# Performance work log

Hardware: AMD Instinct MI355X
Metric: run time of the kernel (lower is better)

The kernel has to match this reference:

```python
import jax, jax.numpy as jnp
import numpy as np

B, L, HID, TRANS = 16384, 512, 768, 128


def setup_inputs() -> dict:
    key = jax.random.key(0)
    ks = jax.random.split(key, 12)
    def lin(k, out_d, in_d):
        kw, kb = jax.random.split(k)
        s = 1.0 / np.sqrt(in_d)
        return (jax.random.uniform(kw, (out_d, in_d), jnp.float32, -s, s),
                jax.random.uniform(kb, (out_d,), jnp.float32, -s, s))
    W_text, b_text = lin(ks[0], TRANS, HID)
    W_label, b_label = lin(ks[1], TRANS, HID)
    W0, b0 = lin(ks[2], TRANS, 2 * TRANS)
    W1, b1 = lin(ks[3], TRANS, TRANS)
    W2, b2 = lin(ks[4], 1, TRANS)
    target = jax.random.randint(ks[5], (B, L), 0, 2, jnp.int32)
    # guarantee every sample has at least one positive label (torch.mean on empty would NaN)
    target = target.at[:, 0].set(1)
    return {
        "text_embed": jax.random.normal(ks[6], (B, HID), jnp.float32),
        "label_embed": jax.random.normal(ks[7], (L, HID), jnp.float32),
        "target": target,
        "perm": jax.random.permutation(ks[8], B).astype(jnp.int32),
        "W_text": W_text, "b_text": b_text,
        "W_label": W_label, "b_label": b_label,
        "W0": W0, "b0": b0, "W1": W1, "b1": b1, "W2": W2, "b2": b2,
    }


def _network(t, l, W_text, b_text, W_label, b_label, W0, b0, W1, b1, W2, b2):
    tt = t @ W_text.T + b_text            # [B, trans]
    ll = l @ W_label.T + b_label          # [B, trans]
    h = jnp.concatenate([tt, ll], axis=1)  # [B, 2*trans]
    h = jax.nn.relu(h @ W0.T + b0)
    h = jax.nn.relu(h @ W1.T + b1)
    return h @ W2.T + b2                  # [B, 1]


def reference(text_embed, label_embed, target, perm,
              W_text, b_text, W_label, b_label, W0, b0, W1, b1, W2, b2):
    # variable-length mean pooling of label embeddings selected by the multi-hot target
    mask = target.astype(text_embed.dtype)                 # [B, L]
    counts = jnp.maximum(mask.sum(axis=1, keepdims=True), 1.0)
    label_feature_y = (mask @ label_embed) / counts        # [B, hid]
    negative_text = text_embed[perm]                       # shuffled negatives
    params = (W_text, b_text, W_label, b_label, W0, b0, W1, b1, W2, b2)
    E_joint = -jnp.mean(jax.nn.softplus(-_network(text_embed, label_feature_y, *params)))
    E_marginal = jnp.mean(jax.nn.softplus(_network(negative_text, label_feature_y, *params)))
    return E_marginal - E_joint
```

## Files before the change

kernel.cpp:

```cpp
#include <hip/hip_runtime.h>
#include <math.h>

#define BATCH 16384
#define LBL   512
#define HID   768
#define TR    128

typedef unsigned long long u64;
typedef unsigned short ushort_t;
typedef __attribute__((ext_vector_type(8))) short short8;
typedef __attribute__((ext_vector_type(4))) float f32x4;

__device__ __forceinline__ ushort_t f2bf(float f){
  unsigned u = __builtin_bit_cast(unsigned, f);
  u += 0x7FFFu + ((u >> 16) & 1u);
  return (ushort_t)(u >> 16);
}
__device__ __forceinline__ float bf2f(ushort_t h){
  unsigned u = ((unsigned)h) << 16;
  return __builtin_bit_cast(float, u);
}
__device__ __forceinline__ float softplusf(float x){
  return fmaxf(x, 0.0f) + log1pf(expf(-fabsf(x)));
}
__device__ __forceinline__ void gload_lds16(const void* g, void* l){
  __builtin_amdgcn_global_load_lds((const __attribute__((address_space(1))) void*)g,
                                   (__attribute__((address_space(3))) void*)l, 16, 0, 0);
}

__global__ __launch_bounds__(256) void k1(
    const float* __restrict__ W0, const float* __restrict__ Wt, const float* __restrict__ Wl,
    const float* __restrict__ bt, const float* __restrict__ bl, const float* __restrict__ b0,
    const float* __restrict__ W1,
    ushort_t* __restrict__ Msw, ushort_t* __restrict__ Qsw, ushort_t* __restrict__ W1B,
    float* __restrict__ KV, float* __restrict__ out){
  __shared__ float sw[TR];
  int bi = blockIdx.x, t = threadIdx.x;
  if (bi < 256){
    int i = bi & 127;
    int isQ = bi >> 7;
    const float* src = isQ ? Wl : Wt;
    ushort_t* dst = isQ ? Qsw : Msw;
    if (t < TR) sw[t] = W0[(size_t)i*256 + isQ*128 + t];
    if (!isQ && t < 128) W1B[i*128 + t] = f2bf(W1[i*128 + t]);
    __syncthreads();
    int c = t;
    float a0 = 0.f, a1 = 0.f, a2 = 0.f;
    #pragma unroll 8
    for (int a = 0; a < 128; a++){
      float w = sw[a];
      const float* r = src + (size_t)a*HID;
      a0 = fmaf(w, r[c], a0);
      a1 = fmaf(w, r[c+256], a1);
      a2 = fmaf(w, r[c+512], a2);
    }
    int c7 = c & 7;
    dst[(((c      )>>3)<<10) + (i<<3) + c7] = f2bf(a0);
    dst[(((c + 256)>>3)<<10) + (i<<3) + c7] = f2bf(a1);
    dst[(((c + 512)>>3)<<10) + (i<<3) + c7] = f2bf(a2);
  } else {
    if (t < TR){
      float s = b0[t];
      const float* r = W0 + (size_t)t*256;
      for (int a = 0; a < 128; a++) s = fmaf(r[a], bt[a], s);
      for (int a = 0; a < 128; a++) s = fmaf(r[128+a], bl[a], s);
      KV[t] = s;
    }
    if (t == 0) out[0] = 0.f;
  }
}

__global__ __launch_bounds__(256) void k2(
    const float* __restrict__ labe, const ushort_t* __restrict__ Qsw,
    const float* __restrict__ T,    const ushort_t* __restrict__ Msw,
    const float* __restrict__ KV,
    ushort_t* __restrict__ Gt, ushort_t* __restrict__ U){
  __shared__ __align__(16) ushort_t Bs[2][8192];
  __shared__ __align__(16) ushort_t As[2][16][72];
  int bi = blockIdx.x, tid = threadIdx.x;
  int lane = tid & 63, wave = tid >> 6;
  int m = lane & 15, q = lane >> 4;
  int arow = tid >> 4, a4 = (tid & 15) * 4;

  if (bi < 32){
    int l0 = bi * 16;
    const float* ap = labe + (size_t)(l0 + arow)*HID + a4;
    float4 ra = *(const float4*)ap;
    {
      const char* gb = (const char*)Qsw;
      char* lb = (char*)&Bs[0][0];
      #pragma unroll
      for (int p = 0; p < 4; p++)
        gload_lds16(gb + p*4096 + tid*16, lb + p*4096 + tid*16);
    }
    f32x4 acc[2] = {{0,0,0,0},{0,0,0,0}};
    for (int c = 0; c < 12; c++){
      int buf = c & 1;
      ushort_t* ad = &As[buf][arow][a4];
      ad[0]=f2bf(ra.x); ad[1]=f2bf(ra.y); ad[2]=f2bf(ra.z); ad[3]=f2bf(ra.w);
      __syncthreads();
      if (c < 11){
        ra = *(const float4*)(ap + (c+1)*64);
        const char* gb = (const char*)Qsw + (size_t)(c+1)*16384;
        char* lb = (char*)&Bs[buf^1][0];
        #pragma unroll
        for (int p = 0; p < 4; p++)
          gload_lds16(gb + p*4096 + tid*16, lb + p*4096 + tid*16);
      }
      #pragma unroll
      for (int kcc = 0; kcc < 2; kcc++){
        short8 a = *(const short8*)&As[buf][m][kcc*32 + q*8];
        #pragma unroll
        for (int ct = 0; ct < 2; ct++){
          int col = wave*32 + ct*16 + m;
          short8 b = *(const short8*)&Bs[buf][(kcc*4 + q)*1024 + col*8];
          acc[ct] = __builtin_amdgcn_mfma_f32_16x16x32_bf16(a, b, acc[ct], 0, 0, 0);
        }
      }
    }
    __syncthreads();
    ushort_t (*GTs)[24] = (ushort_t(*)[24])&Bs[0][0];
    #pragma unroll
    for (int ct = 0; ct < 2; ct++){
      int col = wave*32 + ct*16 + m;
      #pragma unroll
      for (int r = 0; r < 4; r++)
        GTs[col][q*4 + r] = f2bf(acc[ct][r]);
    }
    __syncthreads();
    int gi = tid >> 1, loff = (tid & 1) * 8;
    *(short8*)(Gt + (size_t)gi*LBL + l0 + loff) = *(const short8*)&GTs[gi][loff];
  } else {
    int r0 = (bi - 32) * 16;
    const float* ap = T + (size_t)(r0 + arow)*HID + a4;
    float4 ra = *(const float4*)ap;
    {
      const char* gb = (const char*)Msw;
      char* lb = (char*)&Bs[0][0];
      #pragma unroll
      for (int p = 0; p < 4; p++)
        gload_lds16(gb + p*4096 + tid*16, lb + p*4096 + tid*16);
    }
    f32x4 acc[2] = {{0,0,0,0},{0,0,0,0}};
    for (int c = 0; c < 12; c++){
      int buf = c & 1;
      ushort_t* ad = &As[buf][arow][a4];
      ad[0]=f2bf(ra.x); ad[1]=f2bf(ra.y); ad[2]=f2bf(ra.z); ad[3]=f2bf(ra.w);
      __syncthreads();
      if (c < 11){
        ra = *(const float4*)(ap + (c+1)*64);
        const char* gb = (const char*)Msw + (size_t)(c+1)*16384;
        char* lb = (char*)&Bs[buf^1][0];
        #pragma unroll
        for (int p = 0; p < 4; p++)
          gload_lds16(gb + p*4096 + tid*16, lb + p*4096 + tid*16);
      }
      #pragma unroll
      for (int kcc = 0; kcc < 2; kcc++){
        short8 a = *(const short8*)&As[buf][m][kcc*32 + q*8];
        #pragma unroll
        for (int ct = 0; ct < 2; ct++){
          int col = wave*32 + ct*16 + m;
          short8 b = *(const short8*)&Bs[buf][(kcc*4 + q)*1024 + col*8];
          acc[ct] = __builtin_amdgcn_mfma_f32_16x16x32_bf16(a, b, acc[ct], 0, 0, 0);
        }
      }
    }
    #pragma unroll
    for (int ct = 0; ct < 2; ct++){
      int col = wave*32 + ct*16 + m;
      float kv = KV[col];
      #pragma unroll
      for (int r = 0; r < 4; r++)
        U[(size_t)(r0 + q*4 + r)*TR + col] = f2bf(acc[ct][r] + kv);
    }
  }
}

__global__ __launch_bounds__(256) void k3(const ushort_t* __restrict__ U, const ushort_t* __restrict__ Gt,
                                          const int* __restrict__ tgt, const int* __restrict__ perm,
                                          const ushort_t* __restrict__ W1b, const float* __restrict__ b1,
                                          const float* __restrict__ W2, const float* __restrict__ b2,
                                          float* __restrict__ out){
  __shared__ __align__(16) u64 bits_s8[16*10];
  __shared__ __align__(16) ushort_t h0s[32][136];
  __shared__ float sred[4][2][16][17];
  __shared__ float invs[16];
  __shared__ int   permS[16];

  int tid = threadIdx.x;
  int lane = tid & 63, wave = tid >> 6;
  int m = lane & 15, q = lane >> 4;
  int r0 = blockIdx.x * 16;

  if (tid < 16) permS[tid] = perm[r0 + tid];

  #pragma unroll
  for (int rr = 0; rr < 4; rr++){
    int row = wave*4 + rr;
    const int* rp = tgt + (size_t)(r0 + row)*LBL;
    int v[8];
    #pragma unroll
    for (int c = 0; c < 8; c++) v[c] = rp[c*64 + lane];
    int cnt = 0;
    #pragma unroll
    for (int c = 0; c < 8; c++){
      u64 mm = __ballot(v[c] != 0);
      if (lane == 0){ bits_s8[row*10 + c] = mm; cnt += __popcll(mm); }
    }
    if (lane == 0) invs[row] = 1.0f / (float)(cnt < 1 ? 1 : cnt);
  }
  __syncthreads();

  float up[2][4], un[2][4];
  #pragma unroll
  for (int ct = 0; ct < 2; ct++){
    int col = wave*32 + ct*16 + m;
    #pragma unroll
    for (int r = 0; r < 4; r++){
      int rowl = q*4 + r;
      up[ct][r] = bf2f(U[(size_t)(r0 + rowl)*TR + col]);
      un[ct][r] = bf2f(U[(size_t)permS[rowl]*TR + col]);
    }
  }

  const unsigned char* bits_b = (const unsigned char*)bits_s8;
  f32x4 accV[2] = {{0,0,0,0},{0,0,0,0}};
  const ushort_t* gp[2];
  #pragma unroll
  for (int ct = 0; ct < 2; ct++)
    gp[ct] = Gt + (size_t)(wave*32 + ct*16 + m)*LBL + q*8;
  short8 bcur[2], bnext[2];
  #pragma unroll
  for (int ct = 0; ct < 2; ct++) bcur[ct] = *(const short8*)(gp[ct]);
  int abase = m*80 + q;
  for (int c = 0; c < 16; c++){
    if (c < 15){
      #pragma unroll
      for (int ct = 0; ct < 2; ct++) bnext[ct] = *(const short8*)(gp[ct] + (c+1)*32);
    }
    unsigned bb = bits_b[abase + c*4];
    short8 a;
    #pragma unroll
    for (int j = 0; j < 8; j++) a[j] = (short)(((bb >> j) & 1u) ? 0x3F80 : 0);
    #pragma unroll
    for (int ct = 0; ct < 2; ct++)
      accV[ct] = __builtin_amdgcn_mfma_f32_16x16x32_bf16(a, bcur[ct], accV[ct], 0, 0, 0);
    #pragma unroll
    for (int ct = 0; ct < 2; ct++) bcur[ct] = bnext[ct];
  }

  #pragma unroll
  for (int ct = 0; ct < 2; ct++){
    int col = wave*32 + ct*16 + m;
    #pragma unroll
    for (int r = 0; r < 4; r++){
      int rowl = q*4 + r;
      float v = accV[ct][r] * invs[rowl];
      h0s[rowl][col]      = f2bf(fmaxf(up[ct][r] + v, 0.f));
      h0s[16 + rowl][col] = f2bf(fmaxf(un[ct][r] + v, 0.f));
    }
  }
  __syncthreads();

  float w2c[2], b1c[2];
  #pragma unroll
  for (int ct = 0; ct < 2; ct++){
    int col = wave*32 + ct*16 + m;
    w2c[ct] = W2[col];
    b1c[ct] = b1[col];
  }
  float b2v = b2[0];

  #pragma unroll
  for (int half = 0; half < 2; half++){
    f32x4 accH[2] = {{0,0,0,0},{0,0,0,0}};
    #pragma unroll
    for (int kc = 0; kc < 4; kc++){
      short8 a = *(const short8*)&h0s[half*16 + m][kc*32 + q*8];
      #pragma unroll
      for (int ct = 0; ct < 2; ct++){
        short8 b = *(const short8*)(W1b + (size_t)(wave*32 + ct*16 + m)*TR + kc*32 + q*8);
        accH[ct] = __builtin_amdgcn_mfma_f32_16x16x32_bf16(a, b, accH[ct], 0, 0, 0);
      }
    }
    #pragma unroll
    for (int r = 0; r < 4; r++){
      float sp = 0.f;
      #pragma unroll
      for (int ct = 0; ct < 2; ct++)
        sp = fmaf(w2c[ct], fmaxf(accH[ct][r] + b1c[ct], 0.f), sp);
      sred[wave][half][q*4 + r][m] = sp;
    }
  }
  __syncthreads();

  if (tid < 32){
    int half = tid >> 4, row = tid & 15;
    float s = b2v;
    #pragma unroll
    for (int wx = 0; wx < 4; wx++)
      #pragma unroll
      for (int n = 0; n < 16; n++) s += sred[wx][half][row][n];
    float val = half ? softplusf(s) : softplusf(-s);
    #pragma unroll
    for (int off = 16; off > 0; off >>= 1) val += __shfl_down(val, off);
    if (tid == 0) atomicAdd(out, val * (1.0f / (float)BATCH));
  }
}

extern "C" void kernel_launch(void* const* d_in, const int* in_sizes, int n_in,
                              void* d_out, int out_size, void* d_ws, size_t ws_size,
                              hipStream_t stream){
  const float* text = (const float*)d_in[0];
  const float* labe = (const float*)d_in[1];
  const int*   tgt  = (const int*)  d_in[2];
  const int*   perm = (const int*)  d_in[3];
  const float* Wt   = (const float*)d_in[4];
  const float* bt   = (const float*)d_in[5];
  const float* Wl   = (const float*)d_in[6];
  const float* bl   = (const float*)d_in[7];
  const float* W0   = (const float*)d_in[8];
  const float* b0   = (const float*)d_in[9];
  const float* W1   = (const float*)d_in[10];
  const float* b1   = (const float*)d_in[11];
  const float* W2   = (const float*)d_in[12];
  const float* b2   = (const float*)d_in[13];

  char* wsb = (char*)d_ws;
  size_t off = 0;
  auto alloc = [&](size_t bytes){
    size_t r = off;
    off += (bytes + 255) & ~(size_t)255;
    return r;
  };
  ushort_t* MSW = (ushort_t*)(wsb + alloc((size_t)TR*HID*2));
  ushort_t* QSW = (ushort_t*)(wsb + alloc((size_t)TR*HID*2));
  ushort_t* GT  = (ushort_t*)(wsb + alloc((size_t)TR*LBL*2));
  ushort_t* W1B = (ushort_t*)(wsb + alloc((size_t)TR*TR*2));
  float*    KV  = (float*)   (wsb + alloc((size_t)TR*4));
  ushort_t* U   = (ushort_t*)(wsb + alloc((size_t)BATCH*TR*2));
  (void)ws_size; (void)in_sizes; (void)n_in; (void)out_size;

  k1<<<257, 256, 0, stream>>>(W0, Wt, Wl, bt, bl, b0, W1, MSW, QSW, W1B, KV, (float*)d_out);
  k2<<<1056, 256, 0, stream>>>(labe, QSW, text, MSW, KV, GT, U);
  k3<<<BATCH/16, 256, 0, stream>>>(U, GT, tgt, perm, W1B, b1, W2, b2, (float*)d_out);
}
```

Baseline: 172.8 us.

## Fuse three kernels into one cooperative persistent kernel with grid syncs

Merges the weight-precompute, projection GEMM and MLP/loss kernels into a single cooperative kernel of 512 blocks (32 rows each) separated by two grid-wide barriers. The target bitmask loading now overlaps the weight-preparation phase, and each block keeps its U projection in registers instead of re-reading it. This removes two kernel launch boundaries and their tail effects. In exchange it adds grid.sync costs, caps the grid at two blocks per CU, and serializes the label GEMM onto only 16 blocks. It falls back to the old three-kernel path if occupancy is insufficient.

```diff
diff --git a/kernel.cpp b/kernel.cpp
--- a/kernel.cpp
+++ b/kernel.cpp
@@ -1,4 +1,5 @@
 #include <hip/hip_runtime.h>
+#include <hip/hip_cooperative_groups.h>
 #include <math.h>
 
 #define BATCH 16384
@@ -6,6 +7,8 @@
 #define HID   768
 #define TR    128
 
+namespace cg = cooperative_groups;
+
 typedef unsigned long long u64;
 typedef unsigned short ushort_t;
 typedef __attribute__((ext_vector_type(8))) short short8;
@@ -26,6 +29,286 @@
 __device__ __forceinline__ void gload_lds16(const void* g, void* l){
   __builtin_amdgcn_global_load_lds((const __attribute__((address_space(1))) void*)g,
                                    (__attribute__((address_space(3))) void*)l, 16, 0, 0);
+}
+
+
+__device__ __forceinline__ void gemm768_32(const float* ap, const ushort_t* Bsw,
+                                           ushort_t* As_, ushort_t* Bs_,
+                                           int tid, int wave, int m, int q,
+                                           f32x4 acc[2][2]){
+  int arow = tid >> 3, ak = (tid & 7) * 8;
+  (void)arow; (void)ak;
+  float4 ra0 = *(const float4*)ap;
+  float4 ra1 = *(const float4*)(ap + 4);
+  {
+    const char* gb = (const char*)Bsw;
+    char* lb = (char*)Bs_;
+    #pragma unroll
+    for (int p = 0; p < 4; p++)
+      gload_lds16(gb + p*4096 + tid*16, lb + p*4096 + tid*16);
+  }
+  #pragma unroll
+  for (int rt = 0; rt < 2; rt++)
+    #pragma unroll
+    for (int ct = 0; ct < 2; ct++)
+      acc[rt][ct] = (f32x4){0.f,0.f,0.f,0.f};
+
+  for (int c = 0; c < 12; c++){
+    int buf = c & 1;
+    short8 av;
+    av[0] = (short)f2bf(ra0.x); av[1] = (short)f2bf(ra0.y);
+    av[2] = (short)f2bf(ra0.z); av[3] = (short)f2bf(ra0.w);
+    av[4] = (short)f2bf(ra1.x); av[5] = (short)f2bf(ra1.y);
+    av[6] = (short)f2bf(ra1.z); av[7] = (short)f2bf(ra1.w);
+    *(short8*)(As_ + (size_t)(buf*32 + (tid >> 3))*80 + (tid & 7)*8) = av;
+    __syncthreads();
+    if (c < 11){
+      ra0 = *(const float4*)(ap + (c+1)*64);
+      ra1 = *(const float4*)(ap + (c+1)*64 + 4);
+      const char* gb = (const char*)Bsw + (size_t)(c+1)*16384;
+      char* lb = (char*)(Bs_ + (buf^1)*8192);
+      #pragma unroll
+      for (int p = 0; p < 4; p++)
+        gload_lds16(gb + p*4096 + tid*16, lb + p*4096 + tid*16);
+    }
+    #pragma unroll
+    for (int kcc = 0; kcc < 2; kcc++){
+      short8 bfr[2];
+      #pragma unroll
+      for (int ct = 0; ct < 2; ct++)
+        bfr[ct] = *(const short8*)(Bs_ + buf*8192 + (kcc*4 + q)*1024 + (wave*32 + ct*16 + m)*8);
+      #pragma unroll
+      for (int rt = 0; rt < 2; rt++){
+        short8 a = *(const short8*)(As_ + (size_t)(buf*32 + rt*16 + m)*80 + kcc*32 + q*8);
+        #pragma unroll
+        for (int ct = 0; ct < 2; ct++)
+          acc[rt][ct] = __builtin_amdgcn_mfma_f32_16x16x32_bf16(a, bfr[ct], acc[rt][ct], 0, 0, 0);
+      }
+    }
+  }
+}
+
+__global__ __launch_bounds__(256, 2) void kfused(
+    const float* __restrict__ W0, const float* __restrict__ Wt, const float* __restrict__ Wl,
+    const float* __restrict__ bt, const float* __restrict__ bl, const float* __restrict__ b0,
+    const float* __restrict__ W1, const float* __restrict__ T,  const float* __restrict__ labe,
+    const int* __restrict__ tgt,  const int* __restrict__ perm,
+    const float* __restrict__ b1, const float* __restrict__ W2, const float* __restrict__ b2,
+    ushort_t* __restrict__ Msw, ushort_t* __restrict__ Qsw, ushort_t* __restrict__ W1B,
+    float* __restrict__ KV, ushort_t* __restrict__ Gt, ushort_t* __restrict__ U,
+    float* __restrict__ out){
+  __shared__ __align__(16) char uni[43008];
+  __shared__ __align__(16) u64 bitsS[32*10];
+  __shared__ float invs[32];
+  __shared__ int   permS[32];
+
+  cg::grid_group grid = cg::this_grid();
+  int bi = blockIdx.x, tid = threadIdx.x;
+  int lane = tid & 63, wave = tid >> 6;
+  int m = lane & 15, q = lane >> 4;
+  int r0 = bi * 32;
+  int arow = tid >> 3, ak = (tid & 7) * 8;
+
+  if (tid < 32) permS[tid] = perm[r0 + tid];
+  #pragma unroll
+  for (int rr = 0; rr < 8; rr++){
+    int row = wave*8 + rr;
+    const int* rp = tgt + (size_t)(r0 + row)*LBL;
+    int v[8];
+    #pragma unroll
+    for (int c = 0; c < 8; c++) v[c] = rp[c*64 + lane];
+    int cnt = 0;
+    #pragma unroll
+    for (int c = 0; c < 8; c++){
+      u64 mm = __ballot(v[c] != 0);
+      if (lane == 0){ bitsS[row*10 + c] = mm; cnt += __popcll(mm); }
+    }
+    if (lane == 0) invs[row] = 1.0f / (float)(cnt < 1 ? 1 : cnt);
+  }
+
+  if (bi < 256){
+    int i = bi & 127;
+    int isQ = bi >> 7;
+    const float* src = isQ ? Wl : Wt;
+    ushort_t* dst = isQ ? Qsw : Msw;
+    float* sw = (float*)uni;
+    if (tid < TR) sw[tid] = W0[(size_t)i*256 + isQ*128 + tid];
+    if (!isQ && tid < 128) W1B[i*128 + tid] = f2bf(W1[i*128 + tid]);
+    __syncthreads();
+    int c = tid;
+    float a0 = 0.f, a1 = 0.f, a2 = 0.f;
+    #pragma unroll 8
+    for (int a = 0; a < 128; a++){
+      float w = sw[a];
+      const float* r = src + (size_t)a*HID;
+      a0 = fmaf(w, r[c], a0);
+      a1 = fmaf(w, r[c+256], a1);
+      a2 = fmaf(w, r[c+512], a2);
+    }
+    int c7 = c & 7;
+    dst[(((c      )>>3)<<10) + (i<<3) + c7] = f2bf(a0);
+    dst[(((c + 256)>>3)<<10) + (i<<3) + c7] = f2bf(a1);
+    dst[(((c + 512)>>3)<<10) + (i<<3) + c7] = f2bf(a2);
+  } else if (bi == 256){
+    if (tid < TR){
+      float s = b0[tid];
+      const float* r = W0 + (size_t)tid*256;
+      for (int a = 0; a < 128; a++) s = fmaf(r[a], bt[a], s);
+      for (int a = 0; a < 128; a++) s = fmaf(r[128+a], bl[a], s);
+      KV[tid] = s;
+    }
+    if (tid == 0) out[0] = 0.f;
+  }
+  __threadfence();
+  grid.sync();
+
+  ushort_t* Bs_ = (ushort_t*)uni;
+  ushort_t* As_ = (ushort_t*)(uni + 32768);
+
+  f32x4 accU[2][2];
+  gemm768_32(T + (size_t)(r0 + arow)*HID + ak, Msw, As_, Bs_, tid, wave, m, q, accU);
+
+  float upf[2][2][4];
+  #pragma unroll
+  for (int rt = 0; rt < 2; rt++)
+    #pragma unroll
+    for (int ct = 0; ct < 2; ct++){
+      int col = wave*32 + ct*16 + m;
+      float kv = KV[col];
+      #pragma unroll
+      for (int r = 0; r < 4; r++){
+        upf[rt][ct][r] = accU[rt][ct][r] + kv;
+        U[(size_t)(r0 + rt*16 + q*4 + r)*TR + col] = f2bf(upf[rt][ct][r]);
+      }
+    }
+
+  if (bi < 16){
+    int l0 = bi * 32;
+    f32x4 accG[2][2];
+    __syncthreads();
+    gemm768_32(labe + (size_t)(l0 + arow)*HID + ak, Qsw, As_, Bs_, tid, wave, m, q, accG);
+    __syncthreads();
+    ushort_t (*GTs)[40] = (ushort_t(*)[40])uni;
+    #pragma unroll
+    for (int rt = 0; rt < 2; rt++)
+      #pragma unroll
+      for (int ct = 0; ct < 2; ct++){
+        int col = wave*32 + ct*16 + m;
+        #pragma unroll
+        for (int r = 0; r < 4; r++)
+          GTs[col][rt*16 + q*4 + r] = f2bf(accG[rt][ct][r]);
+      }
+    __syncthreads();
+    int gi = tid >> 1, half = tid & 1;
+    ushort_t* dstp = Gt + (size_t)gi*LBL + l0 + half*16;
+    *(short8*)(dstp)     = *(const short8*)&GTs[gi][half*16];
+    *(short8*)(dstp + 8) = *(const short8*)&GTs[gi][half*16 + 8];
+  }
+  __threadfence();
+  grid.sync();
+
+  ushort_t (*h0s)[136] = (ushort_t(*)[136])uni;
+  float* sred = (float*)(uni + 17408);
+
+  float un[2][2][4];
+  #pragma unroll
+  for (int rt = 0; rt < 2; rt++)
+    #pragma unroll
+    for (int ct = 0; ct < 2; ct++){
+      int col = wave*32 + ct*16 + m;
+      #pragma unroll
+      for (int r = 0; r < 4; r++)
+        un[rt][ct][r] = bf2f(U[(size_t)permS[rt*16 + q*4 + r]*TR + col]);
+    }
+
+  const unsigned char* bits_b = (const unsigned char*)bitsS;
+  f32x4 accV[2][2] = {{{0,0,0,0},{0,0,0,0}},{{0,0,0,0},{0,0,0,0}}};
+  const ushort_t* gp[2];
+  #pragma unroll
+  for (int ct = 0; ct < 2; ct++)
+    gp[ct] = Gt + (size_t)(wave*32 + ct*16 + m)*LBL + q*8;
+  short8 bcur[2], bnext[2];
+  #pragma unroll
+  for (int ct = 0; ct < 2; ct++) bcur[ct] = *(const short8*)(gp[ct]);
+  for (int c = 0; c < 16; c++){
+    if (c < 15){
+      #pragma unroll
+      for (int ct = 0; ct < 2; ct++) bnext[ct] = *(const short8*)(gp[ct] + (c+1)*32);
+    }
+    #pragma unroll
+    for (int rt = 0; rt < 2; rt++){
+      unsigned bb = bits_b[(rt*16 + m)*80 + c*4 + q];
+      short8 a;
+      #pragma unroll
+      for (int j = 0; j < 8; j++) a[j] = (short)(((bb >> j) & 1u) ? 0x3F80 : 0);
+      #pragma unroll
+      for (int ct = 0; ct < 2; ct++)
+        accV[rt][ct] = __builtin_amdgcn_mfma_f32_16x16x32_bf16(a, bcur[ct], accV[rt][ct], 0, 0, 0);
+    }
+    #pragma unroll
+    for (int ct = 0; ct < 2; ct++) bcur[ct] = bnext[ct];
+  }
+
+  __syncthreads();
+  #pragma unroll
+  for (int rt = 0; rt < 2; rt++)
+    #pragma unroll
+    for (int ct = 0; ct < 2; ct++){
+      int col = wave*32 + ct*16 + m;
+      #pragma unroll
+      for (int r = 0; r < 4; r++){
+        int rowl = rt*16 + q*4 + r;
+        float v = accV[rt][ct][r] * invs[rowl];
+        h0s[rowl][col]      = f2bf(fmaxf(upf[rt][ct][r] + v, 0.f));
+        h0s[32 + rowl][col] = f2bf(fmaxf(un[rt][ct][r]  + v, 0.f));
+      }
+    }
+  __syncthreads();
+
+  float w2c[2], b1c[2];
+  #pragma unroll
+  for (int ct = 0; ct < 2; ct++){
+    int col = wave*32 + ct*16 + m;
+    w2c[ct] = W2[col];
+    b1c[ct] = b1[col];
+  }
+  float b2v = b2[0];
+
+  #pragma unroll
+  for (int rt2 = 0; rt2 < 4; rt2++){
+    f32x4 accH[2] = {{0,0,0,0},{0,0,0,0}};
+    #pragma unroll
+    for (int kc = 0; kc < 4; kc++){
+      short8 a = *(const short8*)&h0s[rt2*16 + m][kc*32 + q*8];
+      #pragma unroll
+      for (int ct = 0; ct < 2; ct++){
+        short8 b = *(const short8*)(W1B + (size_t)(wave*32 + ct*16 + m)*TR + kc*32 + q*8);
+        accH[ct] = __builtin_amdgcn_mfma_f32_16x16x32_bf16(a, b, accH[ct], 0, 0, 0);
+      }
+    }
+    #pragma unroll
+    for (int r = 0; r < 4; r++){
+      float sp = 0.f;
+      #pragma unroll
+      for (int ct = 0; ct < 2; ct++)
+        sp = fmaf(w2c[ct], fmaxf(accH[ct][r] + b1c[ct], 0.f), sp);
+      sred[((wave*4 + rt2)*16 + q*4 + r)*17 + m] = sp;
+    }
+  }
+  __syncthreads();
+
+  if (tid < 64){
+    int rt2 = tid >> 4, row = tid & 15;
+    float s = b2v;
+    #pragma unroll
+    for (int wx = 0; wx < 4; wx++)
+      #pragma unroll
+      for (int n = 0; n < 16; n++) s += sred[((wx*4 + rt2)*16 + row)*17 + n];
+    float val = (rt2 < 2) ? softplusf(-s) : softplusf(s);
+    #pragma unroll
+    for (int off = 32; off > 0; off >>= 1) val += __shfl_down(val, off);
+    if (tid == 0) atomicAdd(out, val * (1.0f / (float)BATCH));
+  }
 }
 
 __global__ __launch_bounds__(256) void k1(
@@ -194,7 +477,6 @@
   int r0 = blockIdx.x * 16;
 
   if (tid < 16) permS[tid] = perm[r0 + tid];
-
   #pragma unroll
   for (int rr = 0; rr < 4; rr++){
     int row = wave*4 + rr;
@@ -340,9 +622,24 @@
   ushort_t* W1B = (ushort_t*)(wsb + alloc((size_t)TR*TR*2));
   float*    KV  = (float*)   (wsb + alloc((size_t)TR*4));
   ushort_t* U   = (ushort_t*)(wsb + alloc((size_t)BATCH*TR*2));
+  float*    out = (float*)d_out;
   (void)ws_size; (void)in_sizes; (void)n_in; (void)out_size;
 
-  k1<<<257, 256, 0, stream>>>(W0, Wt, Wl, bt, bl, b0, W1, MSW, QSW, W1B, KV, (float*)d_out);
+  int occ = 0;
+  hipError_t qe = hipOccupancyMaxActiveBlocksPerMultiprocessor(&occ, (const void*)kfused, 256, 0);
+  if (qe == hipSuccess && occ >= 2){
+    void* args[] = {
+      (void*)&W0, (void*)&Wt, (void*)&Wl, (void*)&bt, (void*)&bl, (void*)&b0,
+      (void*)&W1, (void*)&text, (void*)&labe, (void*)&tgt, (void*)&perm,
+      (void*)&b1, (void*)&W2, (void*)&b2,
+      (void*)&MSW, (void*)&QSW, (void*)&W1B, (void*)&KV, (void*)&GT, (void*)&U,
+      (void*)&out
+    };
+    hipError_t e = hipLaunchCooperativeKernel((const void*)kfused, dim3(512), dim3(256), args, 0, stream);
+    if (e == hipSuccess) return;
+  }
+
+  k1<<<257, 256, 0, stream>>>(W0, Wt, Wl, bt, bl, b0, W1, MSW, QSW, W1B, KV, out);
   k2<<<1056, 256, 0, stream>>>(labe, QSW, text, MSW, KV, GT, U);
-  k3<<<BATCH/16, 256, 0, stream>>>(U, GT, tgt, perm, W1B, b1, W2, b2, (float*)d_out);
-}
+  k3<<<BATCH/16, 256, 0, stream>>>(U, GT, tgt, perm, W1B, b1, W2, b2, out);
+}
```

New measurement: 420.6 us. +143.4%, slower.

## Move target bitmask packing into k2 and double row tile to 32 in GEMMs

Applied to the files above, without the earlier changes.

Packing the multi-hot target rows into bitmasks and inverse counts moves from k3 into extra blocks of k2, so it runs concurrently with the text/label projection GEMMs and k3 only reads a compact bitmask. Both the k2 GEMMs and k3 now process 32 rows per block instead of 16, reusing each loaded weight tile across two row tiles of MFMAs. This halves the grid sizes, raises per-block register and LDS use, and adds a workspace round trip for bits and inverse counts.

```diff
diff --git a/kernel.cpp b/kernel.cpp
--- a/kernel.cpp
+++ b/kernel.cpp
@@ -70,162 +70,171 @@
   }
 }
 
+__device__ __forceinline__ void gemm768_32(const float* ap, const ushort_t* Bsw,
+                                           ushort_t* As_, ushort_t* Bs_,
+                                           int tid, int wave, int m, int q,
+                                           f32x4 acc[2][2]){
+  float4 ra0 = *(const float4*)ap;
+  float4 ra1 = *(const float4*)(ap + 4);
+  {
+    const char* gb = (const char*)Bsw;
+    char* lb = (char*)Bs_;
+    #pragma unroll
+    for (int p = 0; p < 4; p++)
+      gload_lds16(gb + p*4096 + tid*16, lb + p*4096 + tid*16);
+  }
+  #pragma unroll
+  for (int rt = 0; rt < 2; rt++)
+    #pragma unroll
+    for (int ct = 0; ct < 2; ct++)
+      acc[rt][ct] = (f32x4){0.f,0.f,0.f,0.f};
+
+  for (int c = 0; c < 12; c++){
+    int buf = c & 1;
+    short8 av;
+    av[0] = (short)f2bf(ra0.x); av[1] = (short)f2bf(ra0.y);
+    av[2] = (short)f2bf(ra0.z); av[3] = (short)f2bf(ra0.w);
+    av[4] = (short)f2bf(ra1.x); av[5] = (short)f2bf(ra1.y);
+    av[6] = (short)f2bf(ra1.z); av[7] = (short)f2bf(ra1.w);
+    *(short8*)(As_ + (size_t)(buf*32 + (tid >> 3))*80 + (tid & 7)*8) = av;
+    __syncthreads();
+    if (c < 11){
+      ra0 = *(const float4*)(ap + (c+1)*64);
+      ra1 = *(const float4*)(ap + (c+1)*64 + 4);
+      const char* gb = (const char*)Bsw + (size_t)(c+1)*16384;
+      char* lb = (char*)(Bs_ + (buf^1)*8192);
+      #pragma unroll
+      for (int p = 0; p < 4; p++)
+        gload_lds16(gb + p*4096 + tid*16, lb + p*4096 + tid*16);
+    }
+    #pragma unroll
+    for (int kcc = 0; kcc < 2; kcc++){
+      short8 bfr[2];
+      #pragma unroll
+      for (int ct = 0; ct < 2; ct++)
+        bfr[ct] = *(const short8*)(Bs_ + buf*8192 + (kcc*4 + q)*1024 + (wave*32 + ct*16 + m)*8);
+      #pragma unroll
+      for (int rt = 0; rt < 2; rt++){
+        short8 a = *(const short8*)(As_ + (size_t)(buf*32 + rt*16 + m)*80 + kcc*32 + q*8);
+        #pragma unroll
+        for (int ct = 0; ct < 2; ct++)
+          acc[rt][ct] = __builtin_amdgcn_mfma_f32_16x16x32_bf16(a, bfr[ct], acc[rt][ct], 0, 0, 0);
+      }
+    }
+  }
+}
+
 __global__ __launch_bounds__(256) void k2(
     const float* __restrict__ labe, const ushort_t* __restrict__ Qsw,
     const float* __restrict__ T,    const ushort_t* __restrict__ Msw,
-    const float* __restrict__ KV,
-    ushort_t* __restrict__ Gt, ushort_t* __restrict__ U){
-  __shared__ __align__(16) ushort_t Bs[2][8192];
-  __shared__ __align__(16) ushort_t As[2][16][72];
+    const float* __restrict__ KV,   const int* __restrict__ tgt,
+    ushort_t* __restrict__ Gt, ushort_t* __restrict__ U,
+    u64* __restrict__ bits, float* __restrict__ inv){
+  __shared__ __align__(16) char uni[43008];
   int bi = blockIdx.x, tid = threadIdx.x;
   int lane = tid & 63, wave = tid >> 6;
   int m = lane & 15, q = lane >> 4;
-  int arow = tid >> 4, a4 = (tid & 15) * 4;
-
-  if (bi < 32){
-    int l0 = bi * 16;
-    const float* ap = labe + (size_t)(l0 + arow)*HID + a4;
-    float4 ra = *(const float4*)ap;
-    {
-      const char* gb = (const char*)Qsw;
-      char* lb = (char*)&Bs[0][0];
-      #pragma unroll
-      for (int p = 0; p < 4; p++)
-        gload_lds16(gb + p*4096 + tid*16, lb + p*4096 + tid*16);
-    }
-    f32x4 acc[2] = {{0,0,0,0},{0,0,0,0}};
-    for (int c = 0; c < 12; c++){
-      int buf = c & 1;
-      ushort_t* ad = &As[buf][arow][a4];
-      ad[0]=f2bf(ra.x); ad[1]=f2bf(ra.y); ad[2]=f2bf(ra.z); ad[3]=f2bf(ra.w);
-      __syncthreads();
-      if (c < 11){
-        ra = *(const float4*)(ap + (c+1)*64);
-        const char* gb = (const char*)Qsw + (size_t)(c+1)*16384;
-        char* lb = (char*)&Bs[buf^1][0];
+  int arow = tid >> 3, ak = (tid & 7) * 8;
+  ushort_t* Bs_ = (ushort_t*)uni;
+  ushort_t* As_ = (ushort_t*)(uni + 32768);
+
+  if (bi < 512){
+    int b0r = bi*32;
+    #pragma unroll
+    for (int rr = 0; rr < 8; rr++){
+      int row = b0r + wave*8 + rr;
+      const int* rp = tgt + (size_t)row*LBL;
+      int v[8];
+      #pragma unroll
+      for (int c = 0; c < 8; c++) v[c] = rp[c*64 + lane];
+      int cnt = 0;
+      #pragma unroll
+      for (int c = 0; c < 8; c++){
+        u64 mm = __ballot(v[c] != 0);
+        if (lane == 0){ bits[(size_t)row*8 + c] = mm; cnt += __popcll(mm); }
+      }
+      if (lane == 0) inv[row] = 1.0f / (float)(cnt < 1 ? 1 : cnt);
+    }
+  } else if (bi < 528){
+    int l0 = (bi - 512) * 32;
+    f32x4 accG[2][2];
+    gemm768_32(labe + (size_t)(l0 + arow)*HID + ak, Qsw, As_, Bs_, tid, wave, m, q, accG);
+    __syncthreads();
+    ushort_t (*GTs)[40] = (ushort_t(*)[40])uni;
+    #pragma unroll
+    for (int rt = 0; rt < 2; rt++)
+      #pragma unroll
+      for (int ct = 0; ct < 2; ct++){
+        int col = wave*32 + ct*16 + m;
         #pragma unroll
-        for (int p = 0; p < 4; p++)
-          gload_lds16(gb + p*4096 + tid*16, lb + p*4096 + tid*16);
-      }
-      #pragma unroll
-      for (int kcc = 0; kcc < 2; kcc++){
-        short8 a = *(const short8*)&As[buf][m][kcc*32 + q*8];
+        for (int r = 0; r < 4; r++)
+          GTs[col][rt*16 + q*4 + r] = f2bf(accG[rt][ct][r]);
+      }
+    __syncthreads();
+    int gi = tid >> 1, half = tid & 1;
+    ushort_t* dstp = Gt + (size_t)gi*LBL + l0 + half*16;
+    *(short8*)(dstp)     = *(const short8*)&GTs[gi][half*16];
+    *(short8*)(dstp + 8) = *(const short8*)&GTs[gi][half*16 + 8];
+  } else {
+    int r0 = (bi - 528) * 32;
+    f32x4 accU[2][2];
+    gemm768_32(T + (size_t)(r0 + arow)*HID + ak, Msw, As_, Bs_, tid, wave, m, q, accU);
+    #pragma unroll
+    for (int rt = 0; rt < 2; rt++)
+      #pragma unroll
+      for (int ct = 0; ct < 2; ct++){
+        int col = wave*32 + ct*16 + m;
+        float kv = KV[col];
         #pragma unroll
-        for (int ct = 0; ct < 2; ct++){
-          int col = wave*32 + ct*16 + m;
-          short8 b = *(const short8*)&Bs[buf][(kcc*4 + q)*1024 + col*8];
-          acc[ct] = __builtin_amdgcn_mfma_f32_16x16x32_bf16(a, b, acc[ct], 0, 0, 0);
-        }
-      }
-    }
-    __syncthreads();
-    ushort_t (*GTs)[24] = (ushort_t(*)[24])&Bs[0][0];
-    #pragma unroll
-    for (int ct = 0; ct < 2; ct++){
-      int col = wave*32 + ct*16 + m;
-      #pragma unroll
-      for (int r = 0; r < 4; r++)
-        GTs[col][q*4 + r] = f2bf(acc[ct][r]);
-    }
-    __syncthreads();
-    int gi = tid >> 1, loff = (tid & 1) * 8;
-    *(short8*)(Gt + (size_t)gi*LBL + l0 + loff) = *(const short8*)&GTs[gi][loff];
-  } else {
-    int r0 = (bi - 32) * 16;
-    const float* ap = T + (size_t)(r0 + arow)*HID + a4;
-    float4 ra = *(const float4*)ap;
-    {
-      const char* gb = (const char*)Msw;
-      char* lb = (char*)&Bs[0][0];
-      #pragma unroll
-      for (int p = 0; p < 4; p++)
-        gload_lds16(gb + p*4096 + tid*16, lb + p*4096 + tid*16);
-    }
-    f32x4 acc[2] = {{0,0,0,0},{0,0,0,0}};
-    for (int c = 0; c < 12; c++){
-      int buf = c & 1;
-      ushort_t* ad = &As[buf][arow][a4];
-      ad[0]=f2bf(ra.x); ad[1]=f2bf(ra.y); ad[2]=f2bf(ra.z); ad[3]=f2bf(ra.w);
-      __syncthreads();
-      if (c < 11){
-        ra = *(const float4*)(ap + (c+1)*64);
-        const char* gb = (const char*)Msw + (size_t)(c+1)*16384;
-        char* lb = (char*)&Bs[buf^1][0];
-        #pragma unroll
-        for (int p = 0; p < 4; p++)
-          gload_lds16(gb + p*4096 + tid*16, lb + p*4096 + tid*16);
-      }
-      #pragma unroll
-      for (int kcc = 0; kcc < 2; kcc++){
-        short8 a = *(const short8*)&As[buf][m][kcc*32 + q*8];
-        #pragma unroll
-        for (int ct = 0; ct < 2; ct++){
-          int col = wave*32 + ct*16 + m;
-          short8 b = *(const short8*)&Bs[buf][(kcc*4 + q)*1024 + col*8];
-          acc[ct] = __builtin_amdgcn_mfma_f32_16x16x32_bf16(a, b, acc[ct], 0, 0, 0);
-        }
-      }
-    }
-    #pragma unroll
-    for (int ct = 0; ct < 2; ct++){
-      int col = wave*32 + ct*16 + m;
-      float kv = KV[col];
-      #pragma unroll
-      for (int r = 0; r < 4; r++)
-        U[(size_t)(r0 + q*4 + r)*TR + col] = f2bf(acc[ct][r] + kv);
-    }
+        for (int r = 0; r < 4; r++)
+          U[(size_t)(r0 + rt*16 + q*4 + r)*TR + col] = f2bf(accU[rt][ct][r] + kv);
+      }
   }
 }
 
 __global__ __launch_bounds__(256) void k3(const ushort_t* __restrict__ U, const ushort_t* __restrict__ Gt,
-                                          const int* __restrict__ tgt, const int* __restrict__ perm,
-                                          const ushort_t* __restrict__ W1b, const float* __restrict__ b1,
-                                          const float* __restrict__ W2, const float* __restrict__ b2,
-                                          float* __restrict__ out){
-  __shared__ __align__(16) u64 bits_s8[16*10];
-  __shared__ __align__(16) ushort_t h0s[32][136];
-  __shared__ float sred[4][2][16][17];
-  __shared__ float invs[16];
-  __shared__ int   permS[16];
+                                          const u64* __restrict__ BITS_, const float* __restrict__ INV,
+                                          const int* __restrict__ perm, const ushort_t* __restrict__ W1b,
+                                          const float* __restrict__ b1, const float* __restrict__ W2,
+                                          const float* __restrict__ b2, float* __restrict__ out){
+  __shared__ __align__(16) u64 bitsS[32*10];
+  __shared__ __align__(16) ushort_t h0s[64][136];
+  __shared__ float sred[4*4*16*17];
+  __shared__ float invs[32];
+  __shared__ int   permS[32];
 
   int tid = threadIdx.x;
   int lane = tid & 63, wave = tid >> 6;
   int m = lane & 15, q = lane >> 4;
-  int r0 = blockIdx.x * 16;
-
-  if (tid < 16) permS[tid] = perm[r0 + tid];
-
-  #pragma unroll
-  for (int rr = 0; rr < 4; rr++){
-    int row = wave*4 + rr;
-    const int* rp = tgt + (size_t)(r0 + row)*LBL;
-    int v[8];
-    #pragma unroll
-    for (int c = 0; c < 8; c++) v[c] = rp[c*64 + lane];
-    int cnt = 0;
-    #pragma unroll
-    for (int c = 0; c < 8; c++){
-      u64 mm = __ballot(v[c] != 0);
-      if (lane == 0){ bits_s8[row*10 + c] = mm; cnt += __popcll(mm); }
-    }
-    if (lane == 0) invs[row] = 1.0f / (float)(cnt < 1 ? 1 : cnt);
+  int r0 = blockIdx.x * 32;
+
+  if (tid < 128){
+    int row = tid >> 2, seg = tid & 3;
+    const int4* src = (const int4*)((const char*)BITS_ + (size_t)(r0+row)*64 + seg*16);
+    *(int4*)((char*)bitsS + row*80 + seg*16) = *src;
+  } else if (tid < 160){
+    invs[tid & 31] = INV[r0 + (tid & 31)];
+  } else if (tid < 192){
+    permS[tid & 31] = perm[r0 + (tid & 31)];
   }
   __syncthreads();
 
-  float up[2][4], un[2][4];
-  #pragma unroll
-  for (int ct = 0; ct < 2; ct++){
-    int col = wave*32 + ct*16 + m;
-    #pragma unroll
-    for (int r = 0; r < 4; r++){
-      int rowl = q*4 + r;
-      up[ct][r] = bf2f(U[(size_t)(r0 + rowl)*TR + col]);
-      un[ct][r] = bf2f(U[(size_t)permS[rowl]*TR + col]);
-    }
-  }
-
-  const unsigned char* bits_b = (const unsigned char*)bits_s8;
-  f32x4 accV[2] = {{0,0,0,0},{0,0,0,0}};
+  float up[2][2][4], un[2][2][4];
+  #pragma unroll
+  for (int rt = 0; rt < 2; rt++)
+    #pragma unroll
+    for (int ct = 0; ct < 2; ct++){
+      int col = wave*32 + ct*16 + m;
+      #pragma unroll
+      for (int r = 0; r < 4; r++){
+        int rowl = rt*16 + q*4 + r;
+        up[rt][ct][r] = bf2f(U[(size_t)(r0 + rowl)*TR + col]);
+        un[rt][ct][r] = bf2f(U[(size_t)permS[rowl]*TR + col]);
+      }
+    }
+
+  const unsigned char* bits_b = (const unsigned char*)bitsS;
+  f32x4 accV[2][2] = {{{0,0,0,0},{0,0,0,0}},{{0,0,0,0},{0,0,0,0}}};
   const ushort_t* gp[2];
   #pragma unroll
   for (int ct = 0; ct < 2; ct++)
@@ -233,34 +242,38 @@
   short8 bcur[2], bnext[2];
   #pragma unroll
   for (int ct = 0; ct < 2; ct++) bcur[ct] = *(const short8*)(gp[ct]);
-  int abase = m*80 + q;
   for (int c = 0; c < 16; c++){
     if (c < 15){
       #pragma unroll
       for (int ct = 0; ct < 2; ct++) bnext[ct] = *(const short8*)(gp[ct] + (c+1)*32);
     }
-    unsigned bb = bits_b[abase + c*4];
-    short8 a;
-    #pragma unroll
-    for (int j = 0; j < 8; j++) a[j] = (short)(((bb >> j) & 1u) ? 0x3F80 : 0);
-    #pragma unroll
-    for (int ct = 0; ct < 2; ct++)
-      accV[ct] = __builtin_amdgcn_mfma_f32_16x16x32_bf16(a, bcur[ct], accV[ct], 0, 0, 0);
+    #pragma unroll
+    for (int rt = 0; rt < 2; rt++){
+      unsigned bb = bits_b[(rt*16 + m)*80 + c*4 + q];
+      short8 a;
+      #pragma unroll
+      for (int j = 0; j < 8; j++) a[j] = (short)(((bb >> j) & 1u) ? 0x3F80 : 0);
+      #pragma unroll
+      for (int ct = 0; ct < 2; ct++)
+        accV[rt][ct] = __builtin_amdgcn_mfma_f32_16x16x32_bf16(a, bcur[ct], accV[rt][ct], 0, 0, 0);
+    }
     #pragma unroll
     for (int ct = 0; ct < 2; ct++) bcur[ct] = bnext[ct];
   }
 
   #pragma unroll
-  for (int ct = 0; ct < 2; ct++){
-    int col = wave*32 + ct*16 + m;
-    #pragma unroll
-    for (int r = 0; r < 4; r++){
-      int rowl = q*4 + r;
-      float v = accV[ct][r] * invs[rowl];
-      h0s[rowl][col]      = f2bf(fmaxf(up[ct][r] + v, 0.f));
-      h0s[16 + rowl][col] = f2bf(fmaxf(un[ct][r] + v, 0.f));
-    }
-  }
+  for (int rt = 0; rt < 2; rt++)
+    #pragma unroll
+    for (int ct = 0; ct < 2; ct++){
+      int col = wave*32 + ct*16 + m;
+      #pragma unroll
+      for (int r = 0; r < 4; r++){
+        int rowl = rt*16 + q*4 + r;
+        float v = accV[rt][ct][r] * invs[rowl];
+        h0s[rowl][col]      = f2bf(fmaxf(up[rt][ct][r] + v, 0.f));
+        h0s[32 + rowl][col] = f2bf(fmaxf(un[rt][ct][r] + v, 0.f));
+      }
+    }
   __syncthreads();
 
   float w2c[2], b1c[2];
@@ -273,11 +286,11 @@
   float b2v = b2[0];
 
   #pragma unroll
-  for (int half = 0; half < 2; half++){
+  for (int rt2 = 0; rt2 < 4; rt2++){
     f32x4 accH[2] = {{0,0,0,0},{0,0,0,0}};
     #pragma unroll
     for (int kc = 0; kc < 4; kc++){
-      short8 a = *(const short8*)&h0s[half*16 + m][kc*32 + q*8];
+      short8 a = *(const short8*)&h0s[rt2*16 + m][kc*32 + q*8];
       #pragma unroll
       for (int ct = 0; ct < 2; ct++){
         short8 b = *(const short8*)(W1b + (size_t)(wave*32 + ct*16 + m)*TR + kc*32 + q*8);
@@ -290,21 +303,21 @@
       #pragma unroll
       for (int ct = 0; ct < 2; ct++)
         sp = fmaf(w2c[ct], fmaxf(accH[ct][r] + b1c[ct], 0.f), sp);
-      sred[wave][half][q*4 + r][m] = sp;
+      sred[((wave*4 + rt2)*16 + q*4 + r)*17 + m] = sp;
     }
   }
   __syncthreads();
 
-  if (tid < 32){
-    int half = tid >> 4, row = tid & 15;
+  if (tid < 64){
+    int rt2 = tid >> 4, row = tid & 15;
     float s = b2v;
     #pragma unroll
     for (int wx = 0; wx < 4; wx++)
       #pragma unroll
-      for (int n = 0; n < 16; n++) s += sred[wx][half][row][n];
-    float val = half ? softplusf(s) : softplusf(-s);
-    #pragma unroll
-    for (int off = 16; off > 0; off >>= 1) val += __shfl_down(val, off);
+      for (int n = 0; n < 16; n++) s += sred[((wx*4 + rt2)*16 + row)*17 + n];
+    float val = (rt2 < 2) ? softplusf(-s) : softplusf(s);
+    #pragma unroll
+    for (int off = 32; off > 0; off >>= 1) val += __shfl_down(val, off);
     if (tid == 0) atomicAdd(out, val * (1.0f / (float)BATCH));
   }
 }
@@ -339,10 +352,13 @@
   ushort_t* GT  = (ushort_t*)(wsb + alloc((size_t)TR*LBL*2));
   ushort_t* W1B = (ushort_t*)(wsb + alloc((size_t)TR*TR*2));
   float*    KV  = (float*)   (wsb + alloc((size_t)TR*4));
+  u64*      BITS= (u64*)     (wsb + alloc((size_t)BATCH*8*8));
+  float*    INV = (float*)   (wsb + alloc((size_t)BATCH*4));
   ushort_t* U   = (ushort_t*)(wsb + alloc((size_t)BATCH*TR*2));
+  float*    out = (float*)d_out;
   (void)ws_size; (void)in_sizes; (void)n_in; (void)out_size;
 
-  k1<<<257, 256, 0, stream>>>(W0, Wt, Wl, bt, bl, b0, W1, MSW, QSW, W1B, KV, (float*)d_out);
-  k2<<<1056, 256, 0, stream>>>(labe, QSW, text, MSW, KV, GT, U);
-  k3<<<BATCH/16, 256, 0, stream>>>(U, GT, tgt, perm, W1B, b1, W2, b2, (float*)d_out);
-}
+  k1<<<257, 256, 0, stream>>>(W0, Wt, Wl, bt, bl, b0, W1, MSW, QSW, W1B, KV, out);
+  k2<<<1040, 256, 0, stream>>>(labe, QSW, text, MSW, KV, tgt, GT, U, BITS, INV);
+  k3<<<512, 256, 0, stream>>>(U, GT, BITS, INV, perm, W1B, b1, W2, b2, out);
+}
```

After: 175.8 us. Within noise of the previous version (+1.7%).
